# Performance work log

Measured on AMD Instinct MI355X. Metric: run time of the kernel, lower is better.

Reference implementation:

```python
import jax, jax.numpy as jnp
import numpy as np

B, DIN, N = 8, 256, 2048  # batch, input_dim (orig node_num), attention nodes (orig seq_len)


def setup_inputs() -> dict:
    key = jax.random.key(0)
    k1, k2, k3, k4 = jax.random.split(key, 4)
    x = jax.random.normal(k1, (B, DIN, N), jnp.float32)
    adj = jax.random.randint(k2, (N, N), 0, 2).astype(jnp.int32)  # binary adjacency
    W = jax.random.normal(k3, (DIN, DIN), jnp.float32) * 0.05      # Linear(D, D, bias=False), stored (out, in)
    a = jax.random.normal(k4, (3 * DIN,), jnp.float32) * 0.05      # Linear(3D, 1, bias=False)
    return {"x": x, "adj": adj, "W": W, "a": a}


def reference(x, adj, W, a):
    # x: (B, D, N) -> permute to (B, N, D); attention is over the N axis
    xt = jnp.transpose(x, (0, 2, 1))
    h = xt @ W.T                                   # (B, N, D)
    sim = jnp.einsum('bid,bjd->bij', h, h)         # (B, N, N) pairwise dot products
    n = adj.shape[0]
    # neighbor mask: adj nonzero, diagonal forced off (mask[:, i] = 0 in the loop)
    m = (adj != 0) & (~jnp.eye(n, dtype=bool))
    # context: the torch loop's weighted_h is independent of its k axis, so
    # context[b, k, i, d] == C[b, i, d] = sum_j m[i,j] * sim[b,i,j] * h[b,j,d]
    C = jnp.einsum('bij,bjd->bid', jnp.where(m[None, :, :], sim, 0.0), h)  # (B, N, D)
    d = h.shape[-1]
    a1, a2, a3 = a[:d], a[d:2 * d], a[2 * d:]
    # a([h_i, h_j, C_j]) = a1.h_i + a2.h_j + a3.C_j  (concat never materialized)
    s_i = h @ a1                                   # (B, N)
    s_j = h @ a2 + C @ a3                          # (B, N)
    scores = jax.nn.leaky_relu(s_i[:, :, None] + s_j[:, None, :], negative_slope=0.2)
    scores = jnp.where(adj[None, :, :] == 0, jnp.float32(-9e15), scores)
    return jax.nn.softmax(scores, axis=-1)         # (B, N, N)
```

## Files before the change

kernel.cpp:

```cpp
#include <hip/hip_runtime.h>
#include <hip/hip_bf16.h>
#include <math.h>

#define Bq   8
#define DINq 256
#define Nq   2048

typedef __attribute__((ext_vector_type(8))) short bf16x8v;
typedef __attribute__((ext_vector_type(4))) float f32x4v;

__device__ __forceinline__ unsigned short f2bf(float f) {
  union { float f; unsigned u; } v; v.f = f;
  unsigned r = v.u + 0x7fffu + ((v.u >> 16) & 1u);
  return (unsigned short)(r >> 16);
}
__device__ __forceinline__ float bf2f(unsigned short h) {
  union { unsigned u; float f; } v; v.u = ((unsigned)h) << 16;
  return v.f;
}

__device__ __forceinline__ void gld_lds16(const void* g, void* l) {
  __builtin_amdgcn_global_load_lds(
      (const __attribute__((address_space(1))) unsigned int*)g,
      (__attribute__((address_space(3))) unsigned int*)l, 16, 0, 0);
}

__device__ __forceinline__ bf16x8v expand_mask(unsigned m8) {
  union { unsigned u[4]; bf16x8v v; } r;
  unsigned lo4 = ((m8 & 0xFu) * 0x204081u) & 0x01010101u;
  unsigned hi4 = (((m8 >> 4) & 0xFu) * 0x204081u) & 0x01010101u;
  r.u[0] = ((lo4 & 0xFFu) | ((lo4 & 0xFF00u) << 8)) * 0x3F80u;
  r.u[1] = (((lo4 >> 16) & 0xFFu) | ((lo4 >> 24) << 16)) * 0x3F80u;
  r.u[2] = ((hi4 & 0xFFu) | ((hi4 & 0xFF00u) << 8)) * 0x3F80u;
  r.u[3] = (((hi4 >> 16) & 0xFFu) | ((hi4 >> 24) << 16)) * 0x3F80u;
  return r.v;
}

__global__ void k_prep(const float* __restrict__ W, const float* __restrict__ a,
                       float* __restrict__ w123) {
  __shared__ float red[3][4][256];
  const int k = threadIdx.x & 255, dq = threadIdx.x >> 8;
  float s1 = 0.f, s2 = 0.f, s3 = 0.f;
  for (int d = dq * 64; d < dq * 64 + 64; ++d) {
    float w = W[d * DINq + k];
    s1 += w * a[d];
    s2 += w * a[DINq + d];
    s3 += w * a[2 * DINq + d];
  }
  red[0][dq][k] = s1; red[1][dq][k] = s2; red[2][dq][k] = s3;
  __syncthreads();
  if (threadIdx.x < 256) {
    w123[k]            = red[0][0][k] + red[0][1][k] + red[0][2][k] + red[0][3][k];
    w123[DINq + k]     = red[1][0][k] + red[1][1][k] + red[1][2][k] + red[1][3][k];
    w123[2 * DINq + k] = red[2][0][k] + red[2][1][k] + red[2][2][k] + red[2][3][k];
  }
}

__global__ void k_transposeW(const float* __restrict__ W, float* __restrict__ WT) {
  int d = blockIdx.x, k = threadIdx.x;
  WT[(size_t)k * DINq + d] = W[(size_t)d * DINq + k];
}

__global__ __launch_bounds__(256, 1) void k_hX(const float* __restrict__ x,
                     const float* __restrict__ WT, const float* __restrict__ w123,
                     unsigned short* __restrict__ Xhi, unsigned short* __restrict__ Xlo,
                     float* __restrict__ tA, float* __restrict__ siA,
                     float* __restrict__ sbA) {
  __shared__ float xs[64][64];
  __shared__ float ws[64][256];
  __shared__ float Tt[64];
  const int tid = threadIdx.x;
  const int iq = tid & 7;
  const int dg = tid >> 3;
  const int i0 = blockIdx.x * 64;
  const int b = blockIdx.y;
  const bool w0 = (tid < 64);

  float acc[8][8];
#pragma unroll
  for (int e = 0; e < 8; ++e)
#pragma unroll
    for (int cc = 0; cc < 8; ++cc) acc[e][cc] = 0.f;
  float p1 = 0.f, p2 = 0.f, p3 = 0.f;

  for (int kc = 0; kc < 4; ++kc) {
    __syncthreads();
#pragma unroll
    for (int l = 0; l < 4; ++l) {
      int c = l * 256 + tid;
      int r = c >> 4, ch = c & 15;
      gld_lds16(&x[((size_t)b * DINq + kc * 64 + r) * Nq + i0 + ch * 4], &xs[r][ch * 4]);
    }
#pragma unroll
    for (int l = 0; l < 16; ++l) {
      int c = l * 256 + tid;
      int r = c >> 6, ch = c & 63;
      gld_lds16(&WT[(size_t)(kc * 64 + r) * DINq + ch * 4], &ws[r][ch * 4]);
    }
    asm volatile("s_waitcnt vmcnt(0)" ::: "memory");
    __syncthreads();
#pragma unroll 4
    for (int kk = 0; kk < 64; ++kk) {
      f32x4v xv0 = *(const f32x4v*)&xs[kk][iq * 8];
      f32x4v xv1 = *(const f32x4v*)&xs[kk][iq * 8 + 4];
      f32x4v wv0 = *(const f32x4v*)&ws[kk][dg * 8];
      f32x4v wv1 = *(const f32x4v*)&ws[kk][dg * 8 + 4];
#pragma unroll
      for (int ii = 0; ii < 4; ++ii) {
#pragma unroll
        for (int cc = 0; cc < 4; ++cc) {
          acc[ii][cc]         += xv0[ii] * wv0[cc];
          acc[ii][cc + 4]     += xv0[ii] * wv1[cc];
          acc[ii + 4][cc]     += xv1[ii] * wv0[cc];
          acc[ii + 4][cc + 4] += xv1[ii] * wv1[cc];
        }
      }
    }
    if (w0) {
#pragma unroll 4
      for (int kk = 0; kk < 64; ++kk) {
        float xv = xs[kk][tid];
        p1 += xv * w123[kc * 64 + kk];
        p2 += xv * w123[DINq + kc * 64 + kk];
        p3 += xv * w123[2 * DINq + kc * 64 + kk];
      }
    }
  }

  if (w0) {
    Tt[tid] = p3;
    tA[(size_t)b * Nq + i0 + tid] = p3;
    siA[(size_t)b * Nq + i0 + tid] = p1;
    sbA[(size_t)b * Nq + i0 + tid] = p2;
  }
  __syncthreads();

  float tv[8];
#pragma unroll
  for (int e = 0; e < 8; ++e) tv[e] = Tt[iq * 8 + e];

#pragma unroll
  for (int cc = 0; cc < 8; ++cc) {
    const int d = dg * 8 + cc;
    unsigned short hv[8], lv[8];
#pragma unroll
    for (int e = 0; e < 8; ++e) {
      float Xv = tv[e] * acc[e][cc];
      unsigned short hs = f2bf(Xv);
      hv[e] = hs;
      lv[e] = f2bf(Xv - bf2f(hs));
    }
    size_t off = ((size_t)b * DINq + d) * Nq + i0 + iq * 8;
    *(ushort4*)&Xhi[off]     = make_ushort4(hv[0], hv[1], hv[2], hv[3]);
    *(ushort4*)&Xhi[off + 4] = make_ushort4(hv[4], hv[5], hv[6], hv[7]);
    *(ushort4*)&Xlo[off]     = make_ushort4(lv[0], lv[1], lv[2], lv[3]);
    *(ushort4*)&Xlo[off + 4] = make_ushort4(lv[4], lv[5], lv[6], lv[7]);
  }
}

__global__ void k_mask(const int* __restrict__ adj, unsigned* __restrict__ bm) {
  int wg = blockIdx.x * 256 + threadIdx.x;
  int i = wg >> 6, w = wg & 63, j0 = w * 32;
  const int4* ap = (const int4*)&adj[(size_t)i * Nq + j0];
  unsigned bits = 0;
#pragma unroll
  for (int q = 0; q < 8; ++q) {
    int4 a = ap[q];
    if (a.x) bits |= 1u << (q * 4);
    if (a.y) bits |= 1u << (q * 4 + 1);
    if (a.z) bits |= 1u << (q * 4 + 2);
    if (a.w) bits |= 1u << (q * 4 + 3);
  }
  bm[wg] = bits;
}

__global__ __launch_bounds__(256, 2) void k_gemm(const unsigned* __restrict__ bm,
                                                 const unsigned short* __restrict__ Xhi,
                                                 const unsigned short* __restrict__ Xlo,
                                                 float* __restrict__ sjp) {
  __shared__ __align__(16) unsigned short Bs[3][2][128 * 32];
  __shared__ unsigned bmlds[256 * 16];
  const int tid = threadIdx.x;
  const int lane = tid & 63;
  const int wave = tid >> 6;
  const int wm = wave >> 1, wc = wave & 1;
  const int wg = blockIdx.x;
  const int xcd = wg & 7;
  const int sub = wg >> 3;
  const int ct = xcd * 2 + (sub & 1);
  const int mt = (sub >> 1) & 7;
  const int ks = sub >> 4;
  const int i0 = mt * 256, c0 = ct * 128, kbase = ks * 512;
  const int r15 = lane & 15, kg = lane >> 4;
  const int kb = 16 * (kg ^ ((r15 >> 1) & 3));

  {
    const int kw0 = kbase >> 5;
#pragma unroll
    for (int n = 0; n < 4; ++n) {
      int idx4 = n * 256 + tid;
      int r = idx4 >> 2, w4 = (idx4 & 3) * 4;
      uint4 v = *(const uint4*)&bm[(size_t)(i0 + r) * 64 + kw0 + w4];
      bmlds[r * 16 + ((w4 + 0) ^ (r & 15))] = v.x;
      bmlds[r * 16 + ((w4 + 1) ^ (r & 15))] = v.y;
      bmlds[r * 16 + ((w4 + 2) ^ (r & 15))] = v.z;
      bmlds[r * 16 + ((w4 + 3) ^ (r & 15))] = v.w;
    }
  }
  __syncthreads();

  f32x4v acc[8][4];
#pragma unroll
  for (int m = 0; m < 8; ++m)
#pragma unroll
    for (int n = 0; n < 4; ++n) acc[m][n] = (f32x4v)0.f;

  auto STAGE = [&](int buf, int t) {
    const int k0 = kbase + t * 32;
#pragma unroll
    for (int l = 0; l < 2; ++l) {
      const int pc = l * 256 + tid;
      const int row = pc >> 2, q = pc & 3;
      const int kc = 8 * (q ^ ((row >> 1) & 3));
      gld_lds16(&Xhi[(size_t)(c0 + row) * Nq + k0 + kc], &Bs[buf][0][pc * 8]);
      gld_lds16(&Xlo[(size_t)(c0 + row) * Nq + k0 + kc], &Bs[buf][1][pc * 8]);
    }
  };

  constexpr int NT = 16;
  STAGE(0, 0);
  STAGE(1, 1);
  int cb = 0, sb2 = 2;
  for (int t = 0; t < NT; ++t) {
    if (t + 1 < NT) {
      asm volatile("s_waitcnt vmcnt(4)" ::: "memory");
    } else {
      asm volatile("s_waitcnt vmcnt(0)" ::: "memory");
    }
    __builtin_amdgcn_sched_barrier(0);
    __builtin_amdgcn_s_barrier();
    __builtin_amdgcn_sched_barrier(0);
    if (t + 2 < NT) STAGE(sb2, t + 2);

    const char* Bh = (const char*)&Bs[cb][0][0];
    const char* Bl = (const char*)&Bs[cb][1][0];
    bf16x8v bfh[4], bfl[4];
#pragma unroll
    for (int n = 0; n < 4; ++n) {
      bfh[n] = *(const bf16x8v*)(Bh + (wc * 64 + n * 16 + r15) * 64 + kb);
      bfl[n] = *(const bf16x8v*)(Bl + (wc * 64 + n * 16 + r15) * 64 + kb);
    }
    const int jb = kbase + t * 32 + kg * 8;
#pragma unroll
    for (int m = 0; m < 8; ++m) {
      const int arow = wm * 128 + m * 16 + r15;
      unsigned wv = bmlds[arow * 16 + (t ^ (arow & 15))];
      unsigned m8 = (wv >> (kg * 8)) & 0xFFu;
      unsigned d = (unsigned)(i0 + arow - jb);
      if (d < 8u) m8 &= ~(1u << d);
      bf16x8v af = expand_mask(m8);
      __builtin_amdgcn_s_setprio(1);
#pragma unroll
      for (int n = 0; n < 4; ++n) {
        acc[m][n] = __builtin_amdgcn_mfma_f32_16x16x32_bf16(af, bfh[n], acc[m][n], 0, 0, 0);
        acc[m][n] = __builtin_amdgcn_mfma_f32_16x16x32_bf16(af, bfl[n], acc[m][n], 0, 0, 0);
      }
      __builtin_amdgcn_s_setprio(0);
    }
    cb = (cb == 2) ? 0 : cb + 1;
    sb2 = (sb2 == 2) ? 0 : sb2 + 1;
  }

  const int b = c0 >> 8;
  const int re = (lane >> 4) * 4, ce = lane & 15;
  float s[8][4];
#pragma unroll
  for (int m = 0; m < 8; ++m)
#pragma unroll
    for (int r = 0; r < 4; ++r) s[m][r] = 0.f;
#pragma unroll
  for (int n = 0; n < 4; ++n) {
    const size_t xrow = (size_t)(c0 + wc * 64 + n * 16 + ce) * Nq;
#pragma unroll
    for (int m = 0; m < 8; ++m) {
      const size_t ib = xrow + i0 + wm * 128 + m * 16 + re;
      ushort4 xh = *(const ushort4*)&Xhi[ib];
      ushort4 xl = *(const ushort4*)&Xlo[ib];
      s[m][0] += acc[m][n][0] * (bf2f(xh.x) + bf2f(xl.x));
      s[m][1] += acc[m][n][1] * (bf2f(xh.y) + bf2f(xl.y));
      s[m][2] += acc[m][n][2] * (bf2f(xh.z) + bf2f(xl.z));
      s[m][3] += acc[m][n][3] * (bf2f(xh.w) + bf2f(xl.w));
    }
  }
#pragma unroll
  for (int o = 1; o < 16; o <<= 1) {
#pragma unroll
    for (int m = 0; m < 8; ++m)
#pragma unroll
      for (int r = 0; r < 4; ++r) s[m][r] += __shfl_xor(s[m][r], o, 64);
  }
  if (ce == 0) {
    const int slice = (ct & 1) * 8 + ks * 2 + wc;
    float* sp = sjp + ((size_t)slice * Bq + b) * Nq;
#pragma unroll
    for (int m = 0; m < 8; ++m)
#pragma unroll
      for (int r = 0; r < 4; ++r)
        sp[i0 + wm * 128 + m * 16 + re + r] = s[m][r];
  }
}

__global__ void k_sjsum(const float* __restrict__ sbA, const float* __restrict__ tA,
                        const float* __restrict__ sjp, float* __restrict__ sjvA) {
  int idx = blockIdx.x * 256 + threadIdx.x;
  float s = 0.f;
#pragma unroll
  for (int sl = 0; sl < 16; ++sl) s += sjp[(size_t)sl * Bq * Nq + idx];
  sjvA[idx] = sbA[idx] + s / tA[idx];
}

__global__ void k_softmax(const unsigned* __restrict__ bm, const float* __restrict__ siA,
                          const float* __restrict__ sjvA, float* __restrict__ out) {
  const int b = blockIdx.y, i = blockIdx.x, tid = threadIdx.x;
  const float siv = siA[(size_t)b * Nq + i];
  const unsigned* brow = bm + (size_t)i * 64;
  const float* sjb = sjvA + (size_t)b * Nq;
  const int bit = tid & 31;
  float sc[8];
  float mx = -3.0e38f;
#pragma unroll
  for (int s = 0; s < 8; ++s) {
    int j = s * 256 + tid;
    float v = siv + sjb[j];
    v = v > 0.f ? v : 0.2f * v;
    unsigned wv = brow[j >> 5];
    v = ((wv >> bit) & 1u) ? v : -9.0e15f;
    sc[s] = v;
    mx = fmaxf(mx, v);
  }
#pragma unroll
  for (int o = 32; o >= 1; o >>= 1) mx = fmaxf(mx, __shfl_xor(mx, o, 64));
  __shared__ float redm[4], reds[4];
  const int wave = tid >> 6, lane = tid & 63;
  if (lane == 0) redm[wave] = mx;
  __syncthreads();
  mx = fmaxf(fmaxf(redm[0], redm[1]), fmaxf(redm[2], redm[3]));
  float sum = 0.f, ex[8];
#pragma unroll
  for (int s = 0; s < 8; ++s) { ex[s] = expf(sc[s] - mx); sum += ex[s]; }
#pragma unroll
  for (int o = 32; o >= 1; o >>= 1) sum += __shfl_xor(sum, o, 64);
  if (lane == 0) reds[wave] = sum;
  __syncthreads();
  sum = reds[0] + reds[1] + reds[2] + reds[3];
  float inv = 1.f / sum;
  float* orow = out + ((size_t)b * Nq + i) * Nq;
#pragma unroll
  for (int s = 0; s < 8; ++s) orow[s * 256 + tid] = ex[s] * inv;
}

extern "C" void kernel_launch(void* const* d_in, const int* in_sizes, int n_in,
                              void* d_out, int out_size, void* d_ws, size_t ws_size,
                              hipStream_t stream) {
  const float* x = (const float*)d_in[0];
  const int* adj = (const int*)d_in[1];
  const float* W = (const float*)d_in[2];
  const float* a = (const float*)d_in[3];
  float* out = (float*)d_out;

  char* ws = (char*)d_ws;
  size_t off = 0;
  auto alloc = [&](size_t bytes) -> void* {
    void* p = ws + off;
    off += (bytes + 255) & ~(size_t)255;
    return p;
  };
  float* w123 = (float*)alloc(3 * DINq * sizeof(float));
  float* WT = (float*)alloc((size_t)DINq * DINq * sizeof(float));
  float* tA = (float*)alloc((size_t)Bq * Nq * sizeof(float));
  float* siA = (float*)alloc((size_t)Bq * Nq * sizeof(float));
  float* sbA = (float*)alloc((size_t)Bq * Nq * sizeof(float));
  float* sjvA = (float*)alloc((size_t)Bq * Nq * sizeof(float));
  float* sjp = (float*)alloc((size_t)16 * Bq * Nq * sizeof(float));
  unsigned short* Xhi = (unsigned short*)alloc((size_t)Nq * Nq * 2);
  unsigned short* Xlo = (unsigned short*)alloc((size_t)Nq * Nq * 2);
  unsigned* bm = (unsigned*)alloc((size_t)Nq * 64 * sizeof(unsigned));

  k_prep<<<dim3(1), dim3(1024), 0, stream>>>(W, a, w123);
  k_transposeW<<<dim3(DINq), dim3(DINq), 0, stream>>>(W, WT);
  k_hX<<<dim3(Nq / 64, Bq), dim3(256), 0, stream>>>(x, WT, w123, Xhi, Xlo, tA, siA, sbA);
  k_mask<<<dim3(Nq * 64 / 256), dim3(256), 0, stream>>>(adj, bm);
  k_gemm<<<dim3(512), dim3(256), 0, stream>>>(bm, Xhi, Xlo, sjp);
  k_sjsum<<<dim3(Bq * Nq / 256), dim3(256), 0, stream>>>(sbA, tA, sjp, sjvA);
  k_softmax<<<dim3(Nq, Bq), dim3(256), 0, stream>>>(bm, siA, sjvA, out);
}
```

Baseline: 136.7 us.

## Halve tile sizes in hX and gemm kernels to raise occupancy and grid size

k_hX now handles 32 columns per block instead of 64, doubling its grid and allowing two blocks per CU. It also caches w123 in LDS and splits the projection reduction across the two wave halves. k_gemm halves its M tile to 128 rows and streams the hi and lo bf16 operands as alternating K stages with a single buffer, doubling grid size to 1024 blocks and targeting 4 blocks per CU. Its output is staged through LDS so global stores are coalesced. The aim is more parallelism and latency hiding, at the cost of more blocks reloading the B tiles and more pipeline iterations.

```diff
diff --git a/kernel.cpp b/kernel.cpp
--- a/kernel.cpp
+++ b/kernel.cpp
@@ -61,24 +61,30 @@
   WT[(size_t)k * DINq + d] = W[(size_t)d * DINq + k];
 }
 
-__global__ __launch_bounds__(256, 1) void k_hX(const float* __restrict__ x,
+__global__ __launch_bounds__(256, 2) void k_hX(const float* __restrict__ x,
                      const float* __restrict__ WT, const float* __restrict__ w123,
                      unsigned short* __restrict__ Xhi, unsigned short* __restrict__ Xlo,
                      float* __restrict__ tA, float* __restrict__ siA,
                      float* __restrict__ sbA) {
-  __shared__ float xs[64][64];
+  __shared__ float xs[64][32];
   __shared__ float ws[64][256];
-  __shared__ float Tt[64];
+  __shared__ float wls[768];
+  __shared__ float Tt[32];
   const int tid = threadIdx.x;
   const int iq = tid & 7;
   const int dg = tid >> 3;
-  const int i0 = blockIdx.x * 64;
+  const int i0 = blockIdx.x * 32;
   const int b = blockIdx.y;
+  const int lane = tid & 63;
   const bool w0 = (tid < 64);
-
-  float acc[8][8];
-#pragma unroll
-  for (int e = 0; e < 8; ++e)
+  const int ti = lane & 31;
+  const int khalf = (lane >> 5) * 32;
+
+  for (int n = tid; n < 768; n += 256) wls[n] = w123[n];
+
+  float acc[4][8];
+#pragma unroll
+  for (int e = 0; e < 4; ++e)
 #pragma unroll
     for (int cc = 0; cc < 8; ++cc) acc[e][cc] = 0.f;
   float p1 = 0.f, p2 = 0.f, p3 = 0.f;
@@ -86,9 +92,9 @@
   for (int kc = 0; kc < 4; ++kc) {
     __syncthreads();
 #pragma unroll
-    for (int l = 0; l < 4; ++l) {
+    for (int l = 0; l < 2; ++l) {
       int c = l * 256 + tid;
-      int r = c >> 4, ch = c & 15;
+      int r = c >> 3, ch = c & 7;
       gld_lds16(&x[((size_t)b * DINq + kc * 64 + r) * Nq + i0 + ch * 4], &xs[r][ch * 4]);
     }
 #pragma unroll
@@ -101,60 +107,61 @@
     __syncthreads();
 #pragma unroll 4
     for (int kk = 0; kk < 64; ++kk) {
-      f32x4v xv0 = *(const f32x4v*)&xs[kk][iq * 8];
-      f32x4v xv1 = *(const f32x4v*)&xs[kk][iq * 8 + 4];
+      f32x4v xv = *(const f32x4v*)&xs[kk][iq * 4];
       f32x4v wv0 = *(const f32x4v*)&ws[kk][dg * 8];
       f32x4v wv1 = *(const f32x4v*)&ws[kk][dg * 8 + 4];
 #pragma unroll
-      for (int ii = 0; ii < 4; ++ii) {
+      for (int e = 0; e < 4; ++e) {
 #pragma unroll
         for (int cc = 0; cc < 4; ++cc) {
-          acc[ii][cc]         += xv0[ii] * wv0[cc];
-          acc[ii][cc + 4]     += xv0[ii] * wv1[cc];
-          acc[ii + 4][cc]     += xv1[ii] * wv0[cc];
-          acc[ii + 4][cc + 4] += xv1[ii] * wv1[cc];
+          acc[e][cc]     += xv[e] * wv0[cc];
+          acc[e][cc + 4] += xv[e] * wv1[cc];
         }
       }
     }
     if (w0) {
 #pragma unroll 4
-      for (int kk = 0; kk < 64; ++kk) {
-        float xv = xs[kk][tid];
-        p1 += xv * w123[kc * 64 + kk];
-        p2 += xv * w123[DINq + kc * 64 + kk];
-        p3 += xv * w123[2 * DINq + kc * 64 + kk];
+      for (int k2 = 0; k2 < 32; ++k2) {
+        int kk = khalf + k2;
+        float xv = xs[kk][ti];
+        p1 += xv * wls[kc * 64 + kk];
+        p2 += xv * wls[256 + kc * 64 + kk];
+        p3 += xv * wls[512 + kc * 64 + kk];
       }
     }
   }
 
   if (w0) {
-    Tt[tid] = p3;
-    tA[(size_t)b * Nq + i0 + tid] = p3;
-    siA[(size_t)b * Nq + i0 + tid] = p1;
-    sbA[(size_t)b * Nq + i0 + tid] = p2;
+    p1 += __shfl_xor(p1, 32, 64);
+    p2 += __shfl_xor(p2, 32, 64);
+    p3 += __shfl_xor(p3, 32, 64);
+    if (lane < 32) {
+      Tt[lane] = p3;
+      tA[(size_t)b * Nq + i0 + lane] = p3;
+      siA[(size_t)b * Nq + i0 + lane] = p1;
+      sbA[(size_t)b * Nq + i0 + lane] = p2;
+    }
   }
   __syncthreads();
 
-  float tv[8];
-#pragma unroll
-  for (int e = 0; e < 8; ++e) tv[e] = Tt[iq * 8 + e];
+  float tv[4];
+#pragma unroll
+  for (int e = 0; e < 4; ++e) tv[e] = Tt[iq * 4 + e];
 
 #pragma unroll
   for (int cc = 0; cc < 8; ++cc) {
     const int d = dg * 8 + cc;
-    unsigned short hv[8], lv[8];
-#pragma unroll
-    for (int e = 0; e < 8; ++e) {
+    unsigned short hv[4], lv[4];
+#pragma unroll
+    for (int e = 0; e < 4; ++e) {
       float Xv = tv[e] * acc[e][cc];
       unsigned short hs = f2bf(Xv);
       hv[e] = hs;
       lv[e] = f2bf(Xv - bf2f(hs));
     }
-    size_t off = ((size_t)b * DINq + d) * Nq + i0 + iq * 8;
-    *(ushort4*)&Xhi[off]     = make_ushort4(hv[0], hv[1], hv[2], hv[3]);
-    *(ushort4*)&Xhi[off + 4] = make_ushort4(hv[4], hv[5], hv[6], hv[7]);
-    *(ushort4*)&Xlo[off]     = make_ushort4(lv[0], lv[1], lv[2], lv[3]);
-    *(ushort4*)&Xlo[off + 4] = make_ushort4(lv[4], lv[5], lv[6], lv[7]);
+    size_t off = ((size_t)b * DINq + d) * Nq + i0 + iq * 4;
+    *(ushort4*)&Xhi[off] = make_ushort4(hv[0], hv[1], hv[2], hv[3]);
+    *(ushort4*)&Xlo[off] = make_ushort4(lv[0], lv[1], lv[2], lv[3]);
   }
 }
 
@@ -174,12 +181,13 @@
   bm[wg] = bits;
 }
 
-__global__ __launch_bounds__(256, 2) void k_gemm(const unsigned* __restrict__ bm,
+__global__ __launch_bounds__(256, 4) void k_gemm(const unsigned* __restrict__ bm,
                                                  const unsigned short* __restrict__ Xhi,
                                                  const unsigned short* __restrict__ Xlo,
                                                  float* __restrict__ sjp) {
-  __shared__ __align__(16) unsigned short Bs[3][2][128 * 32];
-  __shared__ unsigned bmlds[256 * 16];
+  __shared__ __align__(16) unsigned short Bs[3][128 * 32];
+  __shared__ unsigned bmlds[128 * 16];
+  __shared__ float swb[4][64];
   const int tid = threadIdx.x;
   const int lane = tid & 63;
   const int wave = tid >> 6;
@@ -188,16 +196,16 @@
   const int xcd = wg & 7;
   const int sub = wg >> 3;
   const int ct = xcd * 2 + (sub & 1);
-  const int mt = (sub >> 1) & 7;
-  const int ks = sub >> 4;
-  const int i0 = mt * 256, c0 = ct * 128, kbase = ks * 512;
+  const int mt = (sub >> 1) & 15;
+  const int ks = sub >> 5;
+  const int i0 = mt * 128, c0 = ct * 128, kbase = ks * 512;
   const int r15 = lane & 15, kg = lane >> 4;
   const int kb = 16 * (kg ^ ((r15 >> 1) & 3));
 
   {
     const int kw0 = kbase >> 5;
 #pragma unroll
-    for (int n = 0; n < 4; ++n) {
+    for (int n = 0; n < 2; ++n) {
       int idx4 = n * 256 + tid;
       int r = idx4 >> 2, w4 = (idx4 & 3) * 4;
       uint4 v = *(const uint4*)&bm[(size_t)(i0 + r) * 64 + kw0 + w4];
@@ -209,31 +217,31 @@
   }
   __syncthreads();
 
-  f32x4v acc[8][4];
-#pragma unroll
-  for (int m = 0; m < 8; ++m)
+  f32x4v acc[4][4];
+#pragma unroll
+  for (int m = 0; m < 4; ++m)
 #pragma unroll
     for (int n = 0; n < 4; ++n) acc[m][n] = (f32x4v)0.f;
 
   auto STAGE = [&](int buf, int t) {
-    const int k0 = kbase + t * 32;
+    const unsigned short* __restrict__ src = (t & 1) ? Xlo : Xhi;
+    const int k0 = kbase + (t >> 1) * 32;
 #pragma unroll
     for (int l = 0; l < 2; ++l) {
       const int pc = l * 256 + tid;
       const int row = pc >> 2, q = pc & 3;
       const int kc = 8 * (q ^ ((row >> 1) & 3));
-      gld_lds16(&Xhi[(size_t)(c0 + row) * Nq + k0 + kc], &Bs[buf][0][pc * 8]);
-      gld_lds16(&Xlo[(size_t)(c0 + row) * Nq + k0 + kc], &Bs[buf][1][pc * 8]);
+      gld_lds16(&src[(size_t)(c0 + row) * Nq + k0 + kc], &Bs[buf][pc * 8]);
     }
   };
 
-  constexpr int NT = 16;
+  constexpr int NT = 32;
   STAGE(0, 0);
   STAGE(1, 1);
   int cb = 0, sb2 = 2;
   for (int t = 0; t < NT; ++t) {
     if (t + 1 < NT) {
-      asm volatile("s_waitcnt vmcnt(4)" ::: "memory");
+      asm volatile("s_waitcnt vmcnt(2)" ::: "memory");
     } else {
       asm volatile("s_waitcnt vmcnt(0)" ::: "memory");
     }
@@ -242,29 +250,25 @@
     __builtin_amdgcn_sched_barrier(0);
     if (t + 2 < NT) STAGE(sb2, t + 2);
 
-    const char* Bh = (const char*)&Bs[cb][0][0];
-    const char* Bl = (const char*)&Bs[cb][1][0];
-    bf16x8v bfh[4], bfl[4];
-#pragma unroll
-    for (int n = 0; n < 4; ++n) {
-      bfh[n] = *(const bf16x8v*)(Bh + (wc * 64 + n * 16 + r15) * 64 + kb);
-      bfl[n] = *(const bf16x8v*)(Bl + (wc * 64 + n * 16 + r15) * 64 + kb);
-    }
-    const int jb = kbase + t * 32 + kg * 8;
-#pragma unroll
-    for (int m = 0; m < 8; ++m) {
-      const int arow = wm * 128 + m * 16 + r15;
-      unsigned wv = bmlds[arow * 16 + (t ^ (arow & 15))];
+    const char* Bb = (const char*)&Bs[cb][0];
+    bf16x8v bf[4];
+#pragma unroll
+    for (int n = 0; n < 4; ++n)
+      bf[n] = *(const bf16x8v*)(Bb + (wc * 64 + n * 16 + r15) * 64 + kb);
+    const int kch = t >> 1;
+    const int jb = kbase + kch * 32 + kg * 8;
+#pragma unroll
+    for (int m = 0; m < 4; ++m) {
+      const int arow = wm * 64 + m * 16 + r15;
+      unsigned wv = bmlds[arow * 16 + (kch ^ (arow & 15))];
       unsigned m8 = (wv >> (kg * 8)) & 0xFFu;
       unsigned d = (unsigned)(i0 + arow - jb);
       if (d < 8u) m8 &= ~(1u << d);
       bf16x8v af = expand_mask(m8);
       __builtin_amdgcn_s_setprio(1);
 #pragma unroll
-      for (int n = 0; n < 4; ++n) {
-        acc[m][n] = __builtin_amdgcn_mfma_f32_16x16x32_bf16(af, bfh[n], acc[m][n], 0, 0, 0);
-        acc[m][n] = __builtin_amdgcn_mfma_f32_16x16x32_bf16(af, bfl[n], acc[m][n], 0, 0, 0);
-      }
+      for (int n = 0; n < 4; ++n)
+        acc[m][n] = __builtin_amdgcn_mfma_f32_16x16x32_bf16(af, bf[n], acc[m][n], 0, 0, 0);
       __builtin_amdgcn_s_setprio(0);
     }
     cb = (cb == 2) ? 0 : cb + 1;
@@ -273,17 +277,17 @@
 
   const int b = c0 >> 8;
   const int re = (lane >> 4) * 4, ce = lane & 15;
-  float s[8][4];
-#pragma unroll
-  for (int m = 0; m < 8; ++m)
+  float s[4][4];
+#pragma unroll
+  for (int m = 0; m < 4; ++m)
 #pragma unroll
     for (int r = 0; r < 4; ++r) s[m][r] = 0.f;
 #pragma unroll
   for (int n = 0; n < 4; ++n) {
     const size_t xrow = (size_t)(c0 + wc * 64 + n * 16 + ce) * Nq;
 #pragma unroll
-    for (int m = 0; m < 8; ++m) {
-      const size_t ib = xrow + i0 + wm * 128 + m * 16 + re;
+    for (int m = 0; m < 4; ++m) {
+      const size_t ib = xrow + i0 + wm * 64 + m * 16 + re;
       ushort4 xh = *(const ushort4*)&Xhi[ib];
       ushort4 xl = *(const ushort4*)&Xlo[ib];
       s[m][0] += acc[m][n][0] * (bf2f(xh.x) + bf2f(xl.x));
@@ -295,18 +299,22 @@
 #pragma unroll
   for (int o = 1; o < 16; o <<= 1) {
 #pragma unroll
-    for (int m = 0; m < 8; ++m)
+    for (int m = 0; m < 4; ++m)
 #pragma unroll
       for (int r = 0; r < 4; ++r) s[m][r] += __shfl_xor(s[m][r], o, 64);
   }
   if (ce == 0) {
+#pragma unroll
+    for (int m = 0; m < 4; ++m)
+#pragma unroll
+      for (int r = 0; r < 4; ++r)
+        swb[wave][m * 16 + re + r] = s[m][r];
+  }
+  __builtin_amdgcn_s_barrier();
+  {
     const int slice = (ct & 1) * 8 + ks * 2 + wc;
-    float* sp = sjp + ((size_t)slice * Bq + b) * Nq;
-#pragma unroll
-    for (int m = 0; m < 8; ++m)
-#pragma unroll
-      for (int r = 0; r < 4; ++r)
-        sp[i0 + wm * 128 + m * 16 + re + r] = s[m][r];
+    float* sp = sjp + ((size_t)slice * Bq + b) * Nq + i0 + wm * 64;
+    sp[lane] = swb[wave][lane];
   }
 }
 
@@ -388,9 +396,9 @@
 
   k_prep<<<dim3(1), dim3(1024), 0, stream>>>(W, a, w123);
   k_transposeW<<<dim3(DINq), dim3(DINq), 0, stream>>>(W, WT);
-  k_hX<<<dim3(Nq / 64, Bq), dim3(256), 0, stream>>>(x, WT, w123, Xhi, Xlo, tA, siA, sbA);
+  k_hX<<<dim3(Nq / 32, Bq), dim3(256), 0, stream>>>(x, WT, w123, Xhi, Xlo, tA, siA, sbA);
   k_mask<<<dim3(Nq * 64 / 256), dim3(256), 0, stream>>>(adj, bm);
-  k_gemm<<<dim3(512), dim3(256), 0, stream>>>(bm, Xhi, Xlo, sjp);
+  k_gemm<<<dim3(1024), dim3(256), 0, stream>>>(bm, Xhi, Xlo, sjp);
   k_sjsum<<<dim3(Bq * Nq / 256), dim3(256), 0, stream>>>(sbA, tA, sjp, sjvA);
   k_softmax<<<dim3(Nq, Bq), dim3(256), 0, stream>>>(bm, siA, sjvA, out);
 }
```

Measured after the change: 146.7 us. +7.3%, slower.
